# Kernel optimization log

Measured on AMD Instinct MI355X. Metric: run time of the kernel, lower is better.

## Reference

```python
import jax, jax.numpy as jnp
import numpy as np
import math

B, S, D = 4, 2048, 1024
H, DH = 16, 64  # num_heads, head dim (hardcoded 64 in module)


def setup_inputs() -> dict:
    key = jax.random.key(0)
    ks = jax.random.split(key, 5)
    scale = 0.02
    return {
        "x": jax.random.normal(ks[0], (B, S, D), dtype=jnp.float32),
        "W_Q": jax.random.normal(ks[1], (D, H * DH), dtype=jnp.float32) * scale,
        "W_K": jax.random.normal(ks[2], (D, H * DH), dtype=jnp.float32) * scale,
        "W_V": jax.random.normal(ks[3], (D, H * DH), dtype=jnp.float32) * scale,
        "W_O": jax.random.normal(ks[4], (H * DH, D), dtype=jnp.float32) * scale,
        "ln_gamma": jnp.ones((D,), dtype=jnp.float32),
        "ln_beta": jnp.zeros((D,), dtype=jnp.float32),
    }


def reference(x, W_Q, W_K, W_V, W_O, ln_gamma, ln_beta):
    # QKV projections (bias=False Linear: x @ W)
    q = (x @ W_Q).reshape(B, S, H, DH).transpose(0, 2, 1, 3)  # [B,H,S,DH]
    k = (x @ W_K).reshape(B, S, H, DH).transpose(0, 2, 1, 3)
    v = (x @ W_V).reshape(B, S, H, DH).transpose(0, 2, 1, 3)

    # scaled scores with causal mask (upper triangle, diag=1 -> -1e7)
    scores = jnp.einsum("bhsd,bhtd->bhst", q, k) / math.sqrt(DH)  # [B,H,S,S]
    causal = jnp.triu(jnp.ones((S, S), dtype=bool), k=1)
    scores = jnp.where(causal, jnp.float32(-1e7), scores)
    attn = jax.nn.softmax(scores, axis=-1)
    ctx = jnp.einsum("bhst,bhtd->bhsd", attn, v)  # [B,H,S,DH]

    # merge heads, output proj, residual, LayerNorm
    out = ctx.transpose(0, 2, 1, 3).reshape(B, S, H * DH) @ W_O + x
    mu = jnp.mean(out, axis=-1, keepdims=True)
    var = jnp.mean((out - mu) ** 2, axis=-1, keepdims=True)
    out = (out - mu) * jax.lax.rsqrt(var + 1e-5) * ln_gamma + ln_beta
    return out
```

## Files before the change

kernel.cpp:

```cpp
#include <hip/hip_runtime.h>
#include <hip/hip_bf16.h>
#include <cstdint>
#include <cstddef>

#define S_ 2048
#define D_ 1024
#define H_ 16
#define DH_ 64
#define M_ 8192

using bf16 = __bf16;
using bf16x4 = __attribute__((ext_vector_type(4))) __bf16;
using bf16x8 = __attribute__((ext_vector_type(8))) __bf16;
using f32x4 = __attribute__((ext_vector_type(4))) float;
using s16x4 = __attribute__((ext_vector_type(4))) short;

__device__ __forceinline__ void g2lds16(const bf16* g, bf16* l) {
  __builtin_amdgcn_global_load_lds(
      (const __attribute__((address_space(1))) void*)g,
      (__attribute__((address_space(3))) void*)l, 16, 0, 0);
}

__device__ __forceinline__ f32x4 mfma16(bf16x4 a, bf16x4 b, f32x4 c) {
#if __has_builtin(__builtin_amdgcn_mfma_f32_16x16x16_bf16)
  return __builtin_amdgcn_mfma_f32_16x16x16_bf16(a, b, c, 0, 0, 0);
#elif __has_builtin(__builtin_amdgcn_mfma_f32_16x16x16bf16_1k)
  return __builtin_amdgcn_mfma_f32_16x16x16bf16_1k(
      __builtin_bit_cast(s16x4, a), __builtin_bit_cast(s16x4, b), c, 0, 0, 0);
#else
  f32x4 d;
  asm("v_mfma_f32_16x16x16_bf16 %0, %1, %2, %3"
      : "=v"(d)
      : "v"(a), "v"(b), "v"(c));
  return d;
#endif
}

__global__ __launch_bounds__(256) void cvt_all_kernel(
    const float* __restrict__ x, const float* __restrict__ w0,
    const float* __restrict__ w1, const float* __restrict__ w2,
    const float* __restrict__ w3, bf16* __restrict__ xb,
    bf16* __restrict__ o0, bf16* __restrict__ o1, bf16* __restrict__ o2,
    bf16* __restrict__ o3) {
  __shared__ float tile[32][33];
  int bx = blockIdx.x;
  int tid = threadIdx.x;
  if (bx < 4096) {
    size_t i = ((size_t)bx * 256 + tid) * 8;
    float4 a = *(const float4*)(x + i);
    float4 b = *(const float4*)(x + i + 4);
    bf16x8 o;
    o[0] = (bf16)a.x; o[1] = (bf16)a.y; o[2] = (bf16)a.z; o[3] = (bf16)a.w;
    o[4] = (bf16)b.x; o[5] = (bf16)b.y; o[6] = (bf16)b.z; o[7] = (bf16)b.w;
    *(bf16x8*)(xb + i) = o;
    return;
  }
  int wb = bx - 4096;
  int wsel = wb >> 10; wb &= 1023;
  const float* W; bf16* O;
  switch (wsel) {
    case 0: W = w0; O = o0; break;
    case 1: W = w1; O = o1; break;
    case 2: W = w2; O = o2; break;
    default: W = w3; O = o3; break;
  }
  int n0 = (wb & 31) * 32;
  int k0 = (wb >> 5) * 32;
#pragma unroll
  for (int i = 0; i < 4; ++i) {
    int e = tid + i * 256; int rr = e >> 5, cc = e & 31;
    tile[rr][cc] = W[(size_t)(k0 + rr) * 1024 + n0 + cc];
  }
  __syncthreads();
#pragma unroll
  for (int i = 0; i < 4; ++i) {
    int e = tid + i * 256; int rr = e >> 5, cc = e & 31;
    O[(size_t)(n0 + rr) * 1024 + k0 + cc] = (bf16)tile[cc][rr];
  }
}

template <int MODE>
__global__ __launch_bounds__(512, 4) void gemm_kernel(
    const bf16* __restrict__ A,
    const bf16* __restrict__ Bt0, const bf16* __restrict__ Bt1,
    const bf16* __restrict__ Bt2,
    bf16* __restrict__ Qo, bf16* __restrict__ Ko, bf16* __restrict__ Vto) {
  extern __shared__ float4 smem4[];
  bf16* smem = (bf16*)smem4;

  constexpr int NWG = (MODE == 0) ? 768 : 256;
  constexpr int CPX = NWG / 8;
  constexpr int NBN = (MODE == 0) ? 12 : 4;
  const int wg = ((int)blockIdx.x & 7) * CPX + ((int)blockIdx.x >> 3);
  const int bn = wg % NBN, bm = wg / NBN;

  const bf16* Bt;
  int n0full = 0, wsel = 0;
  if constexpr (MODE == 0) {
    wsel = bn >> 2;
    Bt = (wsel == 0) ? Bt0 : (wsel == 1 ? Bt1 : Bt2);
    n0full = (bn & 3) * 256;
  } else {
    Bt = Bt0;
    n0full = bn * 256;
  }

  const int tid = threadIdx.x;
  const int wave = tid >> 6, lane = tid & 63;
  const int quad = lane >> 4, r = lane & 15;
  const int wm = (wave >> 2) * 64, wn = (wave & 3) * 64;

  const int lrow = lane >> 2;
  const int lcol = ((lane & 3) ^ ((lrow >> 1) & 3)) * 8;
  const int am = bm * 128 + wave * 16 + lrow;
  const bf16 *pA, *pB1, *pB2;
  if constexpr (MODE == 0) {
    pA = A + (size_t)am * 1024 + lcol;
  } else {
    pA = A + (size_t)(am >> 11) * (16 * (size_t)S_ * DH_) +
         (size_t)(am & 2047) * 64 + lcol;
  }
  const int bnr = n0full + wave * 16 + lrow;
  pB1 = Bt + (size_t)bnr * 1024 + lcol;
  pB2 = Bt + (size_t)(bnr + 128) * 1024 + lcol;
  constexpr ptrdiff_t dSum = (MODE == 0) ? 64 : (ptrdiff_t)S_ * DH_;
  ptrdiff_t dTog = 32;

  const int oA = wave * 512;
  const int oB1 = 4096 + wave * 512;
  const int oB2 = 8192 + wave * 512;

  auto stage = [&](bf16* base) {
    g2lds16(pA, base + oA);
    g2lds16(pB1, base + oB1);
    g2lds16(pB2, base + oB2);
    pA += dTog; dTog = dSum - dTog;
    pB1 += 32; pB2 += 32;
  };

  f32x4 acc[4][4];
  const f32x4 zero = {0.f, 0.f, 0.f, 0.f};
#pragma unroll
  for (int i = 0; i < 4; ++i)
#pragma unroll
    for (int j = 0; j < 4; ++j) acc[i][j] = zero;

  const int x0 = (quad ^ ((r >> 1) & 3)) * 8;
  const int raB = (wm + r) * 32;
  const int rbB = (wn + r) * 32;

  auto phase = [&](const bf16* buf) {
    const bf16* bA = buf;
    const bf16* bB = buf + 4096;
    bf16x8 af[4], bg[4];
#pragma unroll
    for (int i = 0; i < 4; ++i)
      af[i] = *(const bf16x8*)(bA + raB + i * 512 + x0);
#pragma unroll
    for (int j = 0; j < 4; ++j)
      bg[j] = *(const bf16x8*)(bB + rbB + j * 512 + x0);
    __builtin_amdgcn_s_setprio(1);
#pragma unroll
    for (int i = 0; i < 4; ++i)
#pragma unroll
      for (int j = 0; j < 4; ++j)
        acc[i][j] = __builtin_amdgcn_mfma_f32_16x16x32_bf16(af[i], bg[j],
                                                            acc[i][j], 0, 0, 0);
    __builtin_amdgcn_s_setprio(0);
  };

  bf16* b0 = smem;
  bf16* b1 = smem + 12288;
  bf16* b2 = smem + 24576;

  stage(b0);
  stage(b1);

#pragma unroll 1
  for (int kt = 0; kt < 30; kt += 3) {
    asm volatile("s_waitcnt vmcnt(3)\n\ts_barrier" ::: "memory");
    stage(b2);
    phase(b0);
    asm volatile("s_waitcnt vmcnt(3)\n\ts_barrier" ::: "memory");
    stage(b0);
    phase(b1);
    asm volatile("s_waitcnt vmcnt(3)\n\ts_barrier" ::: "memory");
    stage(b1);
    phase(b2);
  }
  asm volatile("s_waitcnt vmcnt(3)\n\ts_barrier" ::: "memory");
  phase(b0);
  asm volatile("s_waitcnt vmcnt(0)\n\ts_barrier" ::: "memory");
  phase(b1);

  const int mB = bm * 128 + wm + quad * 4;
  if constexpr (MODE == 0) {
    if (wsel < 2) {
      bf16* dst = (wsel == 0) ? Qo : Ko;
#pragma unroll
      for (int i = 0; i < 4; ++i) {
#pragma unroll
        for (int j = 0; j < 4; ++j) {
          int n = n0full + wn + j * 16 + r;
          int h = n >> 6, dh = n & 63;
#pragma unroll
          for (int g = 0; g < 4; ++g) {
            int m = mB + i * 16 + g;
            int b = m >> 11, s = m & 2047;
            dst[((size_t)(b * H_ + h) * S_ + s) * DH_ + dh] =
                (bf16)acc[i][j][g];
          }
        }
      }
    } else {
#pragma unroll
      for (int i = 0; i < 4; ++i) {
        int m = mB + i * 16;
        int b = m >> 11, s = m & 2047;
#pragma unroll
        for (int j = 0; j < 4; ++j) {
          int n = n0full + wn + j * 16 + r;
          int h = n >> 6, dh = n & 63;
          bf16x4 pk;
#pragma unroll
          for (int g = 0; g < 4; ++g) pk[g] = (bf16)acc[i][j][g];
          *(bf16x4*)(Vto + ((size_t)(b * H_ + h) * DH_ + dh) * S_ + s) = pk;
        }
      }
    }
  } else {
#pragma unroll
    for (int i = 0; i < 4; ++i) {
#pragma unroll
      for (int j = 0; j < 4; ++j) {
        int n = bn * 256 + wn + j * 16 + r;
#pragma unroll
        for (int g = 0; g < 4; ++g) {
          int m = mB + i * 16 + g;
          Qo[(size_t)m * 1024 + n] = (bf16)acc[i][j][g];
        }
      }
    }
  }
}

__global__ __launch_bounds__(512, 4) void attn_kernel(const bf16* __restrict__ Qb,
                                                      const bf16* __restrict__ Kb,
                                                      const bf16* __restrict__ Vtb,
                                                      bf16* __restrict__ ctx) {
  __shared__ __align__(16) bf16 smK[2][2][64 * 64];
  __shared__ __align__(16) bf16 smV[2][2][64 * 64];
  const int bx = blockIdx.x;
  const int bh = bx & 63;
  const int i256 = (bx < 256) ? (7 - (bx >> 6)) : ((bx - 256) >> 6);
  const bf16* Qh = Qb + (size_t)bh * S_ * DH_;
  const bf16* Kh = Kb + (size_t)bh * S_ * DH_;
  const bf16* Vh = Vtb + (size_t)bh * DH_ * S_;
  bf16* Ch = ctx + (size_t)bh * S_ * DH_;
  const int tid = threadIdx.x, wave = tid >> 6, lane = tid & 63;
  const int quad = lane >> 4, r = lane & 15;
  const int r7 = r & 7;
  const int wrow = wave * 8 + (lane >> 3);
  const int gcol = ((lane & 7) ^ (lane >> 3)) * 8;
  const f32x4 zero = {0.f, 0.f, 0.f, 0.f};
  const int xk0 = (quad ^ r7) * 8, xk1 = ((quad + 4) ^ r7) * 8;

  const int q0w = i256 * 256 + wave * 32;
  const int numkt = 4 * i256 + 4;
  const int NU = numkt >> 1;
  const int lastkt = q0w >> 6;

  bf16x8 qf[2][2];
  const float qsc = 0.125f * 1.44269504f;
#pragma unroll
  for (int qg = 0; qg < 2; ++qg)
#pragma unroll
    for (int hh = 0; hh < 2; ++hh) {
      bf16x8 q = *(const bf16x8*)(Qh + (size_t)(q0w + qg * 16 + r) * DH_ +
                                  hh * 32 + quad * 8);
#pragma unroll
      for (int i = 0; i < 8; ++i) q[i] = (bf16)((float)q[i] * qsc);
      qf[qg][hh] = q;
    }

  f32x4 lacc[2] = {zero, zero};
  f32x4 oacc[2][4];
#pragma unroll
  for (int qg = 0; qg < 2; ++qg)
#pragma unroll
    for (int tn = 0; tn < 4; ++tn) oacc[qg][tn] = zero;

  auto STAGE = [&](int u, int b) {
#pragma unroll
    for (int sub = 0; sub < 2; ++sub) {
      const int kt = 2 * u + sub;
      g2lds16(Kh + (size_t)(kt * 64 + wrow) * DH_ + gcol,
              &smK[b][sub][wave * 512]);
      g2lds16(Vh + (size_t)wrow * S_ + kt * 64 + gcol,
              &smV[b][sub][wave * 512]);
    }
  };

  STAGE(0, 0);
  asm volatile("s_waitcnt vmcnt(0)\n\ts_barrier" ::: "memory");

#pragma unroll 1
  for (int u = 0; u < NU; ++u) {
    const int b = u & 1;
    if (u + 1 < NU) STAGE(u + 1, b ^ 1);
#pragma unroll
    for (int sub = 0; sub < 2; ++sub) {
      const int kt = 2 * u + sub;
      if (kt <= lastkt) {
        const int kv0 = kt * 64;
        const bf16* kb = &smK[b][sub][0];
        const bf16* vb = &smV[b][sub][0];

        f32x4 s[2][4];
#pragma unroll
        for (int t = 0; t < 4; ++t) {
          bf16x8 kf0 = *(const bf16x8*)(kb + (t * 16 + r) * 64 + xk0);
          bf16x8 kf1 = *(const bf16x8*)(kb + (t * 16 + r) * 64 + xk1);
#pragma unroll
          for (int qg = 0; qg < 2; ++qg) {
            f32x4 z = __builtin_amdgcn_mfma_f32_16x16x32_bf16(kf0, qf[qg][0],
                                                              zero, 0, 0, 0);
            s[qg][t] = __builtin_amdgcn_mfma_f32_16x16x32_bf16(kf1, qf[qg][1],
                                                               z, 0, 0, 0);
          }
        }
        if (kt == lastkt) {
#pragma unroll
          for (int qg = 0; qg < 2; ++qg) {
            const int q = q0w + qg * 16 + r;
#pragma unroll
            for (int t = 0; t < 4; ++t) {
              const int kv = kv0 + t * 16 + quad * 4;
#pragma unroll
              for (int g = 0; g < 4; ++g)
                if (kv + g > q) s[qg][t][g] = -1e30f;
            }
          }
        }
#pragma unroll
        for (int t = 0; t < 4; ++t) {
          bf16x4 pa[2];
#pragma unroll
          for (int qg = 0; qg < 2; ++qg) {
#pragma unroll
            for (int g = 0; g < 4; ++g)
              s[qg][t][g] = __builtin_amdgcn_exp2f(s[qg][t][g]);
            lacc[qg] += s[qg][t];
            bf16x4 pk;
#pragma unroll
            for (int g = 0; g < 4; ++g) pk[g] = (bf16)s[qg][t][g];
            pa[qg] = pk;
          }
#pragma unroll
          for (int tn = 0; tn < 4; ++tn) {
            bf16x4 vf = *(const bf16x4*)(
                vb + (tn * 16 + r) * 64 +
                ((2 * t + (quad >> 1)) ^ r7) * 8 + (quad & 1) * 4);
            oacc[0][tn] = mfma16(pa[0], vf, oacc[0][tn]);
            oacc[1][tn] = mfma16(pa[1], vf, oacc[1][tn]);
          }
        }
      }
    }
    asm volatile("s_waitcnt vmcnt(0) lgkmcnt(0)\n\ts_barrier" ::: "memory");
  }

#pragma unroll
  for (int qg = 0; qg < 2; ++qg) {
    float rs = (lacc[qg][0] + lacc[qg][1]) + (lacc[qg][2] + lacc[qg][3]);
    rs += __shfl_xor(rs, 16, 64);
    rs += __shfl_xor(rs, 32, 64);
    const float inv = 1.f / rs;
    f32x4 ib;
#pragma unroll
    for (int g = 0; g < 4; ++g) ib[g] = __shfl(inv, quad * 4 + g, 64);
#pragma unroll
    for (int tn = 0; tn < 4; ++tn) {
      f32x4 ov = oacc[qg][tn] * ib;
#pragma unroll
      for (int g = 0; g < 4; ++g)
        Ch[(size_t)(q0w + qg * 16 + quad * 4 + g) * DH_ + tn * 16 + r] =
            (bf16)ov[g];
    }
  }
}

__global__ __launch_bounds__(256) void ln_kernel(float* __restrict__ out,
                                                 const bf16* __restrict__ pb,
                                                 const float* __restrict__ x,
                                                 const float* __restrict__ gamma,
                                                 const float* __restrict__ beta) {
  __shared__ float red[8];
  size_t row = blockIdx.x;
  int tid = threadIdx.x;
  float4 xv = ((const float4*)(x + row * 1024))[tid];
  bf16x4 pv = *(const bf16x4*)(pb + row * 1024 + tid * 4);
  float v0 = xv.x + (float)pv[0];
  float v1 = xv.y + (float)pv[1];
  float v2 = xv.z + (float)pv[2];
  float v3 = xv.w + (float)pv[3];
  float s1 = v0 + v1 + v2 + v3;
  float s2 = v0 * v0 + v1 * v1 + v2 * v2 + v3 * v3;
#pragma unroll
  for (int o = 1; o < 64; o <<= 1) {
    s1 += __shfl_xor(s1, o, 64);
    s2 += __shfl_xor(s2, o, 64);
  }
  int wave = tid >> 6, lane = tid & 63;
  if (lane == 0) { red[wave] = s1; red[4 + wave] = s2; }
  __syncthreads();
  s1 = red[0] + red[1] + red[2] + red[3];
  s2 = red[4] + red[5] + red[6] + red[7];
  float mean = s1 * (1.f / 1024.f);
  float var = s2 * (1.f / 1024.f) - mean * mean;
  float rstd = rsqrtf(var + 1e-5f);
  float4 g = ((const float4*)gamma)[tid];
  float4 b = ((const float4*)beta)[tid];
  float4 o;
  o.x = (v0 - mean) * rstd * g.x + b.x;
  o.y = (v1 - mean) * rstd * g.y + b.y;
  o.z = (v2 - mean) * rstd * g.z + b.z;
  o.w = (v3 - mean) * rstd * g.w + b.w;
  ((float4*)(out + row * 1024))[tid] = o;
}

extern "C" void kernel_launch(void* const* d_in, const int* in_sizes, int n_in,
                              void* d_out, int out_size, void* d_ws,
                              size_t ws_size, hipStream_t stream) {
  (void)in_sizes; (void)n_in; (void)out_size; (void)ws_size;
  const float* x  = (const float*)d_in[0];
  const float* WQ = (const float*)d_in[1];
  const float* WK = (const float*)d_in[2];
  const float* WV = (const float*)d_in[3];
  const float* WO = (const float*)d_in[4];
  const float* gamma = (const float*)d_in[5];
  const float* beta  = (const float*)d_in[6];
  float* out = (float*)d_out;

  bf16* ws = (bf16*)d_ws;
  const size_t MD = (size_t)M_ * D_;
  const size_t WW = (size_t)D_ * D_;
  bf16* xb   = ws;
  bf16* wqt  = xb + MD;
  bf16* wkt  = wqt + WW;
  bf16* wvt  = wkt + WW;
  bf16* wot  = wvt + WW;
  bf16* Qb   = wot + WW;
  bf16* Kb   = Qb + MD;
  bf16* Vtb  = Kb + MD;
  bf16* ctxb = Vtb + MD;
  bf16* projb = Qb;

  constexpr int GEMM_LDS = 3 * 24 * 1024;
  static bool s_attr = false;
  if (!s_attr) {
    s_attr = true;
    (void)hipFuncSetAttribute(reinterpret_cast<const void*>(gemm_kernel<0>),
                              hipFuncAttributeMaxDynamicSharedMemorySize,
                              GEMM_LDS);
    (void)hipFuncSetAttribute(reinterpret_cast<const void*>(gemm_kernel<1>),
                              hipFuncAttributeMaxDynamicSharedMemorySize,
                              GEMM_LDS);
  }

  cvt_all_kernel<<<dim3(8192), dim3(256), 0, stream>>>(
      x, WQ, WK, WV, WO, xb, wqt, wkt, wvt, wot);
  gemm_kernel<0><<<dim3(768), dim3(512), GEMM_LDS, stream>>>(
      xb, wqt, wkt, wvt, Qb, Kb, Vtb);
  attn_kernel<<<dim3(512), dim3(512), 0, stream>>>(Qb, Kb, Vtb, ctxb);
  gemm_kernel<1><<<dim3(256), dim3(512), GEMM_LDS, stream>>>(
      ctxb, wot, nullptr, nullptr, projb, nullptr, nullptr);
  ln_kernel<<<dim3(8192), dim3(256), 0, stream>>>(out, projb, x, gamma, beta);
}
```

Measured before the change: 237.8 us.

## Split QKV GEMM into 4-wave kernel with larger per-wave tiles; LN reads bf16 x

The QKV projection GEMM becomes its own kernel with 256 threads. Each wave now computes a 128x64 output tile (8x4 MFMA accumulators) instead of 64x64, which raises register-level reuse of the A and B fragments and lowers LDS read traffic per MFMA. The cost is more registers per wave and fewer waves per block to hide latency. Separately, LayerNorm reads the bf16 copy of x for the residual instead of fp32, halving that read but adding rounding error to the residual.

Result: no change. 238.6 us (+0.4%).

```diff
diff --git a/kernel.cpp b/kernel.cpp
--- a/kernel.cpp
+++ b/kernel.cpp
@@ -79,31 +79,144 @@
   }
 }
 
-template <int MODE>
-__global__ __launch_bounds__(512, 4) void gemm_kernel(
-    const bf16* __restrict__ A,
-    const bf16* __restrict__ Bt0, const bf16* __restrict__ Bt1,
-    const bf16* __restrict__ Bt2,
+__global__ __launch_bounds__(256, 2) void gemmA_kernel(
+    const bf16* __restrict__ A, const bf16* __restrict__ Bt0,
+    const bf16* __restrict__ Bt1, const bf16* __restrict__ Bt2,
     bf16* __restrict__ Qo, bf16* __restrict__ Ko, bf16* __restrict__ Vto) {
   extern __shared__ float4 smem4[];
   bf16* smem = (bf16*)smem4;
 
-  constexpr int NWG = (MODE == 0) ? 768 : 256;
-  constexpr int CPX = NWG / 8;
-  constexpr int NBN = (MODE == 0) ? 12 : 4;
-  const int wg = ((int)blockIdx.x & 7) * CPX + ((int)blockIdx.x >> 3);
-  const int bn = wg % NBN, bm = wg / NBN;
-
-  const bf16* Bt;
-  int n0full = 0, wsel = 0;
-  if constexpr (MODE == 0) {
-    wsel = bn >> 2;
-    Bt = (wsel == 0) ? Bt0 : (wsel == 1 ? Bt1 : Bt2);
-    n0full = (bn & 3) * 256;
+  const int wg = ((int)blockIdx.x & 7) * 96 + ((int)blockIdx.x >> 3);
+  const int bn = wg % 12, bm = wg / 12;
+  const int wsel = bn >> 2;
+  const bf16* Bt = (wsel == 0) ? Bt0 : (wsel == 1 ? Bt1 : Bt2);
+  const int n0 = (bn & 3) * 256;
+
+  const int tid = threadIdx.x;
+  const int wave = tid >> 6, lane = tid & 63;
+  const int quad = lane >> 4, r = lane & 15;
+
+  const int lrow = lane >> 2;
+  const int lcol = ((lane & 3) ^ ((lrow >> 1) & 3)) * 8;
+  const int am0 = bm * 128 + wave * 32 + lrow;
+  const bf16* pA0 = A + (size_t)am0 * 1024 + lcol;
+  const bf16* pA1 = A + (size_t)(am0 + 16) * 1024 + lcol;
+  const int bnr = n0 + wave * 64 + lrow;
+  const bf16* pB0 = Bt + (size_t)bnr * 1024 + lcol;
+  const bf16* pB1 = Bt + (size_t)(bnr + 16) * 1024 + lcol;
+  const bf16* pB2 = Bt + (size_t)(bnr + 32) * 1024 + lcol;
+  const bf16* pB3 = Bt + (size_t)(bnr + 48) * 1024 + lcol;
+
+  const int oA0 = wave * 1024, oA1 = wave * 1024 + 512;
+  const int oB0 = 4096 + wave * 2048;
+
+  auto stage = [&](bf16* base) {
+    g2lds16(pA0, base + oA0); pA0 += 32;
+    g2lds16(pA1, base + oA1); pA1 += 32;
+    g2lds16(pB0, base + oB0); pB0 += 32;
+    g2lds16(pB1, base + oB0 + 512); pB1 += 32;
+    g2lds16(pB2, base + oB0 + 1024); pB2 += 32;
+    g2lds16(pB3, base + oB0 + 1536); pB3 += 32;
+  };
+
+  f32x4 acc[8][4];
+  const f32x4 zero = {0.f, 0.f, 0.f, 0.f};
+#pragma unroll
+  for (int i = 0; i < 8; ++i)
+#pragma unroll
+    for (int j = 0; j < 4; ++j) acc[i][j] = zero;
+
+  const int x0 = (quad ^ ((r >> 1) & 3)) * 8;
+  const int raB = r * 32;
+  const int rbB = 4096 + (wave * 64 + r) * 32;
+
+  auto phase = [&](const bf16* buf) {
+    bf16x8 af[8], bg[4];
+#pragma unroll
+    for (int i = 0; i < 8; ++i)
+      af[i] = *(const bf16x8*)(buf + raB + i * 512 + x0);
+#pragma unroll
+    for (int j = 0; j < 4; ++j)
+      bg[j] = *(const bf16x8*)(buf + rbB + j * 512 + x0);
+    __builtin_amdgcn_s_setprio(1);
+#pragma unroll
+    for (int i = 0; i < 8; ++i)
+#pragma unroll
+      for (int j = 0; j < 4; ++j)
+        acc[i][j] = __builtin_amdgcn_mfma_f32_16x16x32_bf16(af[i], bg[j],
+                                                            acc[i][j], 0, 0, 0);
+    __builtin_amdgcn_s_setprio(0);
+  };
+
+  bf16* b0 = smem;
+  bf16* b1 = smem + 12288;
+  bf16* b2 = smem + 24576;
+
+  stage(b0);
+  stage(b1);
+
+#pragma unroll 1
+  for (int kt = 0; kt < 30; kt += 3) {
+    asm volatile("s_waitcnt vmcnt(6)\n\ts_barrier" ::: "memory");
+    stage(b2);
+    phase(b0);
+    asm volatile("s_waitcnt vmcnt(6)\n\ts_barrier" ::: "memory");
+    stage(b0);
+    phase(b1);
+    asm volatile("s_waitcnt vmcnt(6)\n\ts_barrier" ::: "memory");
+    stage(b1);
+    phase(b2);
+  }
+  asm volatile("s_waitcnt vmcnt(6)\n\ts_barrier" ::: "memory");
+  phase(b0);
+  asm volatile("s_waitcnt vmcnt(0)\n\ts_barrier" ::: "memory");
+  phase(b1);
+
+  const int mB = bm * 128 + quad * 4;
+  if (wsel < 2) {
+    bf16* dst = (wsel == 0) ? Qo : Ko;
+#pragma unroll
+    for (int i = 0; i < 8; ++i) {
+#pragma unroll
+      for (int j = 0; j < 4; ++j) {
+        int n = n0 + wave * 64 + j * 16 + r;
+        int h = n >> 6, dh = n & 63;
+#pragma unroll
+        for (int g = 0; g < 4; ++g) {
+          int m = mB + i * 16 + g;
+          int b = m >> 11, s = m & 2047;
+          dst[((size_t)(b * H_ + h) * S_ + s) * DH_ + dh] = (bf16)acc[i][j][g];
+        }
+      }
+    }
   } else {
-    Bt = Bt0;
-    n0full = bn * 256;
-  }
+#pragma unroll
+    for (int i = 0; i < 8; ++i) {
+      int m = mB + i * 16;
+      int b = m >> 11, s = m & 2047;
+#pragma unroll
+      for (int j = 0; j < 4; ++j) {
+        int n = n0 + wave * 64 + j * 16 + r;
+        int h = n >> 6, dh = n & 63;
+        bf16x4 pk;
+#pragma unroll
+        for (int g = 0; g < 4; ++g) pk[g] = (bf16)acc[i][j][g];
+        *(bf16x4*)(Vto + ((size_t)(b * H_ + h) * DH_ + dh) * S_ + s) = pk;
+      }
+    }
+  }
+}
+
+__global__ __launch_bounds__(512, 4) void gemmB_kernel(
+    const bf16* __restrict__ A, const bf16* __restrict__ Bt0,
+    bf16* __restrict__ Qo) {
+  extern __shared__ float4 smem4[];
+  bf16* smem = (bf16*)smem4;
+
+  const int wg = ((int)blockIdx.x & 7) * 32 + ((int)blockIdx.x >> 3);
+  const int bn = wg % 4, bm = wg / 4;
+  const bf16* Bt = Bt0;
+  const int n0full = bn * 256;
 
   const int tid = threadIdx.x;
   const int wave = tid >> 6, lane = tid & 63;
@@ -113,17 +226,12 @@
   const int lrow = lane >> 2;
   const int lcol = ((lane & 3) ^ ((lrow >> 1) & 3)) * 8;
   const int am = bm * 128 + wave * 16 + lrow;
-  const bf16 *pA, *pB1, *pB2;
-  if constexpr (MODE == 0) {
-    pA = A + (size_t)am * 1024 + lcol;
-  } else {
-    pA = A + (size_t)(am >> 11) * (16 * (size_t)S_ * DH_) +
-         (size_t)(am & 2047) * 64 + lcol;
-  }
+  const bf16* pA = A + (size_t)(am >> 11) * (16 * (size_t)S_ * DH_) +
+                   (size_t)(am & 2047) * 64 + lcol;
   const int bnr = n0full + wave * 16 + lrow;
-  pB1 = Bt + (size_t)bnr * 1024 + lcol;
-  pB2 = Bt + (size_t)(bnr + 128) * 1024 + lcol;
-  constexpr ptrdiff_t dSum = (MODE == 0) ? 64 : (ptrdiff_t)S_ * DH_;
+  const bf16* pB1 = Bt + (size_t)bnr * 1024 + lcol;
+  const bf16* pB2 = Bt + (size_t)(bnr + 128) * 1024 + lcol;
+  constexpr ptrdiff_t dSum = (ptrdiff_t)S_ * DH_;
   ptrdiff_t dTog = 32;
 
   const int oA = wave * 512;
@@ -194,51 +302,15 @@
   phase(b1);
 
   const int mB = bm * 128 + wm + quad * 4;
-  if constexpr (MODE == 0) {
-    if (wsel < 2) {
-      bf16* dst = (wsel == 0) ? Qo : Ko;
-#pragma unroll
-      for (int i = 0; i < 4; ++i) {
-#pragma unroll
-        for (int j = 0; j < 4; ++j) {
-          int n = n0full + wn + j * 16 + r;
-          int h = n >> 6, dh = n & 63;
-#pragma unroll
-          for (int g = 0; g < 4; ++g) {
-            int m = mB + i * 16 + g;
-            int b = m >> 11, s = m & 2047;
-            dst[((size_t)(b * H_ + h) * S_ + s) * DH_ + dh] =
-                (bf16)acc[i][j][g];
-          }
-        }
-      }
-    } else {
-#pragma unroll
-      for (int i = 0; i < 4; ++i) {
-        int m = mB + i * 16;
-        int b = m >> 11, s = m & 2047;
-#pragma unroll
-        for (int j = 0; j < 4; ++j) {
-          int n = n0full + wn + j * 16 + r;
-          int h = n >> 6, dh = n & 63;
-          bf16x4 pk;
-#pragma unroll
-          for (int g = 0; g < 4; ++g) pk[g] = (bf16)acc[i][j][g];
-          *(bf16x4*)(Vto + ((size_t)(b * H_ + h) * DH_ + dh) * S_ + s) = pk;
-        }
-      }
-    }
-  } else {
-#pragma unroll
-    for (int i = 0; i < 4; ++i) {
-#pragma unroll
-      for (int j = 0; j < 4; ++j) {
-        int n = bn * 256 + wn + j * 16 + r;
-#pragma unroll
-        for (int g = 0; g < 4; ++g) {
-          int m = mB + i * 16 + g;
-          Qo[(size_t)m * 1024 + n] = (bf16)acc[i][j][g];
-        }
+#pragma unroll
+  for (int i = 0; i < 4; ++i) {
+#pragma unroll
+    for (int j = 0; j < 4; ++j) {
+      int n = n0full + wn + j * 16 + r;
+#pragma unroll
+      for (int g = 0; g < 4; ++g) {
+        int m = mB + i * 16 + g;
+        Qo[(size_t)m * 1024 + n] = (bf16)acc[i][j][g];
       }
     }
   }
@@ -392,18 +464,18 @@
 
 __global__ __launch_bounds__(256) void ln_kernel(float* __restrict__ out,
                                                  const bf16* __restrict__ pb,
-                                                 const float* __restrict__ x,
+                                                 const bf16* __restrict__ xb,
                                                  const float* __restrict__ gamma,
                                                  const float* __restrict__ beta) {
   __shared__ float red[8];
   size_t row = blockIdx.x;
   int tid = threadIdx.x;
-  float4 xv = ((const float4*)(x + row * 1024))[tid];
+  bf16x4 xv = *(const bf16x4*)(xb + row * 1024 + tid * 4);
   bf16x4 pv = *(const bf16x4*)(pb + row * 1024 + tid * 4);
-  float v0 = xv.x + (float)pv[0];
-  float v1 = xv.y + (float)pv[1];
-  float v2 = xv.z + (float)pv[2];
-  float v3 = xv.w + (float)pv[3];
+  float v0 = (float)xv[0] + (float)pv[0];
+  float v1 = (float)xv[1] + (float)pv[1];
+  float v2 = (float)xv[2] + (float)pv[2];
+  float v3 = (float)xv[3] + (float)pv[3];
   float s1 = v0 + v1 + v2 + v3;
   float s2 = v0 * v0 + v1 * v1 + v2 * v2 + v3 * v3;
 #pragma unroll
@@ -460,20 +532,20 @@
   static bool s_attr = false;
   if (!s_attr) {
     s_attr = true;
-    (void)hipFuncSetAttribute(reinterpret_cast<const void*>(gemm_kernel<0>),
+    (void)hipFuncSetAttribute(reinterpret_cast<const void*>(gemmA_kernel),
                               hipFuncAttributeMaxDynamicSharedMemorySize,
                               GEMM_LDS);
-    (void)hipFuncSetAttribute(reinterpret_cast<const void*>(gemm_kernel<1>),
+    (void)hipFuncSetAttribute(reinterpret_cast<const void*>(gemmB_kernel),
                               hipFuncAttributeMaxDynamicSharedMemorySize,
                               GEMM_LDS);
   }
 
   cvt_all_kernel<<<dim3(8192), dim3(256), 0, stream>>>(
       x, WQ, WK, WV, WO, xb, wqt, wkt, wvt, wot);
-  gemm_kernel<0><<<dim3(768), dim3(512), GEMM_LDS, stream>>>(
+  gemmA_kernel<<<dim3(768), dim3(256), GEMM_LDS, stream>>>(
       xb, wqt, wkt, wvt, Qb, Kb, Vtb);
   attn_kernel<<<dim3(512), dim3(512), 0, stream>>>(Qb, Kb, Vtb, ctxb);
-  gemm_kernel<1><<<dim3(256), dim3(512), GEMM_LDS, stream>>>(
-      ctxb, wot, nullptr, nullptr, projb, nullptr, nullptr);
-  ln_kernel<<<dim3(8192), dim3(256), 0, stream>>>(out, projb, x, gamma, beta);
-}
+  gemmB_kernel<<<dim3(256), dim3(512), GEMM_LDS, stream>>>(
+      ctxb, wot, projb);
+  ln_kernel<<<dim3(8192), dim3(256), 0, stream>>>(out, projb, xb, gamma, beta);
+}
```
